# Performance work log

Measured on AMD Instinct MI355X. Metric: run time of the kernel, lower is better.

Reference implementation:

```python
import jax, jax.numpy as jnp
import numpy as np

B, T, C = 2, 2048, 2048
NH, NKV = 16, 4
HD = C // NH  # 128
DFF = 4 * C


def rmsnorm(x):
    eps = jnp.finfo(x.dtype).eps
    return x * jax.lax.rsqrt(jnp.mean(jnp.square(x), axis=-1, keepdims=True) + eps)


def rotary(x, cos, sin):
    # x: [B,T,H,HD], cos/sin: [1,T,1,HD//2]
    d = x.shape[-1] // 2
    x1, x2 = x[..., :d], x[..., d:]
    return jnp.concatenate([x1 * cos + x2 * sin, -x1 * sin + x2 * cos], axis=-1)


def setup_inputs() -> dict:
    key = jax.random.key(0)
    ks = jax.random.split(key, 8)
    x = jax.random.normal(ks[0], (B, T, C), jnp.float32)
    inv_freq = 1.0 / (10000.0 ** (jnp.arange(HD // 2, dtype=jnp.float32) / (HD // 2)))
    ang = jnp.arange(T, dtype=jnp.float32)[:, None] * inv_freq[None, :]  # [T, HD//2]
    cos = jnp.cos(ang)[None, :, None, :]
    sin = jnp.sin(ang)[None, :, None, :]
    s = 0.02
    wq = jax.random.normal(ks[1], (C, NH * HD), jnp.float32) * s
    wk = jax.random.normal(ks[2], (C, NKV * HD), jnp.float32) * s
    wv = jax.random.normal(ks[3], (C, NKV * HD), jnp.float32) * s
    wo = jax.random.normal(ks[4], (C, C), jnp.float32) * s
    w_fc = jax.random.normal(ks[5], (C, DFF), jnp.float32) * s
    w_proj = jax.random.normal(ks[6], (DFF, C), jnp.float32) * s
    return {"x": x, "cos": cos, "sin": sin, "wq": wq, "wk": wk, "wv": wv,
            "wo": wo, "w_fc": w_fc, "w_proj": w_proj}


def reference(x, cos, sin, wq, wk, wv, wo, w_fc, w_proj):
    # --- attention sublayer (pre-norm residual) ---
    h = rmsnorm(x)
    q = (h @ wq).reshape(B, T, NH, HD)
    k = (h @ wk).reshape(B, T, NKV, HD)
    v = (h @ wv).reshape(B, T, NKV, HD)
    q = rmsnorm(rotary(q, cos, sin))
    k = rmsnorm(rotary(k, cos, sin))
    rep = NH // NKV
    k = jnp.repeat(k, rep, axis=2)  # [B,T,NH,HD]
    v = jnp.repeat(v, rep, axis=2)
    scale = 1.0 / np.sqrt(HD)
    scores = jnp.einsum('bqhd,bkhd->bhqk', q, k) * scale
    causal = jnp.tril(jnp.ones((T, T), dtype=bool))
    scores = jnp.where(causal[None, None], scores, jnp.finfo(scores.dtype).min)
    attn = jax.nn.softmax(scores, axis=-1)
    y = jnp.einsum('bhqk,bkhd->bqhd', attn, v).reshape(B, T, C)
    x = x + y @ wo
    # --- MLP sublayer (relu^2) ---
    h = rmsnorm(x)
    h = jnp.square(jax.nn.relu(h @ w_fc))
    x = x + h @ w_proj
    return x
```

## Files before the change

### kernel.cpp

```cpp
#include <hip/hip_runtime.h>
#include <cstdint>
#include <cstddef>


#define B_    2
#define T_    2048
#define C_    2048
#define NH_   16
#define NKV_  4
#define HD_   128
#define DFF_  8192
#define EPS_  1.1920928955078125e-07f

typedef short          bf16x8 __attribute__((ext_vector_type(8)));
typedef float          f32x4  __attribute__((ext_vector_type(4)));
typedef unsigned short u16;
typedef unsigned short u16x8  __attribute__((ext_vector_type(8)));
typedef unsigned short u16x4  __attribute__((ext_vector_type(4)));

__device__ __forceinline__ u16 f2bf(float f) {
    unsigned u = __float_as_uint(f);
    unsigned r = u + 0x7fffu + ((u >> 16) & 1u);
    return (u16)(r >> 16);
}
__device__ __forceinline__ float bf2f(u16 u) {
    return __uint_as_float((unsigned)u << 16);
}

__device__ __forceinline__ void load_lds16(const void* g, void* l) {
    __builtin_amdgcn_global_load_lds(
        (__attribute__((address_space(1))) void*)(g),
        (__attribute__((address_space(3))) void*)(l), 16, 0, 0);
}

__device__ __forceinline__ unsigned lds_addr(const void* p) {
    return (unsigned)(unsigned long long)(__attribute__((address_space(3))) const void*)p;
}

struct TD  { const float* src; u16* dst; int K, N, boff; };
struct TD6 { TD t[6]; };

__global__ void transpose_cast_all(TD6 d) {
    int bid = blockIdx.x;
    int di = 0;
    for (int i = 5; i > 0; --i) if (bid >= d.t[i].boff) { di = i; break; }
    const float* src = d.t[di].src;
    u16* dst = d.t[di].dst;
    int K = d.t[di].K, N = d.t[di].N;
    int lb = bid - d.t[di].boff;
    int nx = N >> 5;
    int n0 = (lb % nx) * 32;
    int k0 = (lb / nx) * 32;

    __shared__ float tile[32][33];
    int tx = threadIdx.x & 31;
    int ty = threadIdx.x >> 5;
    for (int j = 0; j < 4; ++j)
        tile[ty + j * 8][tx] = src[(size_t)(k0 + ty + j * 8) * N + n0 + tx];
    __syncthreads();
    for (int j = 0; j < 4; ++j)
        dst[(size_t)(n0 + ty + j * 8) * K + k0 + tx] = f2bf(tile[tx][ty + j * 8]);
}

__global__ void transpose_v(const u16* __restrict__ vb, u16* __restrict__ Vt) {
    int bx   = blockIdx.x;
    int dblk = bx & 1;
    int t0   = (bx >> 1) * 32;
    int kvh  = blockIdx.y, b = blockIdx.z;
    int dl   = threadIdx.x & 63;
    int tc   = threadIdx.x >> 6;
    int d    = dblk * 64 + dl;
    u16x8 v8;
    for (int j = 0; j < 8; ++j) {
        int t = t0 + tc * 8 + j;
        v8[j] = vb[((size_t)(b * T_ + t) * NKV_ + kvh) * HD_ + d];
    }
    *(u16x8*)(Vt + ((size_t)((b * NKV_ + kvh) * HD_ + d)) * T_ + t0 + tc * 8) = v8;
}

__global__ void rmsnorm_rows(const float* __restrict__ x, u16* __restrict__ out) {
    int row = blockIdx.x;
    const float4* xr = (const float4*)(x + (size_t)row * C_);
    float4 a = xr[threadIdx.x];
    float4 b = xr[threadIdx.x + 256];
    float ss = a.x * a.x + a.y * a.y + a.z * a.z + a.w * a.w
             + b.x * b.x + b.y * b.y + b.z * b.z + b.w * b.w;
    for (int m = 1; m < 64; m <<= 1) ss += __shfl_xor(ss, m, 64);
    __shared__ float part[4];
    if ((threadIdx.x & 63) == 0) part[threadIdx.x >> 6] = ss;
    __syncthreads();
    float tot = part[0] + part[1] + part[2] + part[3];
    float sc = rsqrtf(tot * (1.0f / C_) + EPS_);
    u16x4 o1, o2;
    o1[0] = f2bf(a.x * sc); o1[1] = f2bf(a.y * sc); o1[2] = f2bf(a.z * sc); o1[3] = f2bf(a.w * sc);
    o2[0] = f2bf(b.x * sc); o2[1] = f2bf(b.y * sc); o2[2] = f2bf(b.z * sc); o2[3] = f2bf(b.w * sc);
    u16x4* orow = (u16x4*)(out + (size_t)row * C_);
    orow[threadIdx.x]       = o1;
    orow[threadIdx.x + 256] = o2;
}

__global__ void reduce_rms(const float* __restrict__ x, const u16* __restrict__ p0,
                           const u16* __restrict__ p1, float* __restrict__ x2,
                           u16* __restrict__ hout) {
    int row = blockIdx.x;
    const float4* xr = (const float4*)(x + (size_t)row * C_);
    const u16x4* a0 = (const u16x4*)(p0 + (size_t)row * C_);
    const u16x4* a1 = (const u16x4*)(p1 + (size_t)row * C_);
    float4 v[2];
    float ss = 0.f;
    for (int h = 0; h < 2; ++h) {
        int idx = threadIdx.x + h * 256;
        float4 xv = xr[idx];
        u16x4 b0 = a0[idx], b1 = a1[idx];
        v[h].x = xv.x + bf2f(b0[0]) + bf2f(b1[0]);
        v[h].y = xv.y + bf2f(b0[1]) + bf2f(b1[1]);
        v[h].z = xv.z + bf2f(b0[2]) + bf2f(b1[2]);
        v[h].w = xv.w + bf2f(b0[3]) + bf2f(b1[3]);
        ss += v[h].x * v[h].x + v[h].y * v[h].y + v[h].z * v[h].z + v[h].w * v[h].w;
    }
    for (int m = 1; m < 64; m <<= 1) ss += __shfl_xor(ss, m, 64);
    __shared__ float part[4];
    if ((threadIdx.x & 63) == 0) part[threadIdx.x >> 6] = ss;
    __syncthreads();
    float tot = part[0] + part[1] + part[2] + part[3];
    float sc = rsqrtf(tot * (1.0f / C_) + EPS_);
    float4* x2r = (float4*)(x2 + (size_t)row * C_);
    u16x4* hr   = (u16x4*)(hout + (size_t)row * C_);
    for (int h = 0; h < 2; ++h) {
        int idx = threadIdx.x + h * 256;
        x2r[idx] = v[h];
        u16x4 o;
        o[0] = f2bf(v[h].x * sc); o[1] = f2bf(v[h].y * sc);
        o[2] = f2bf(v[h].z * sc); o[3] = f2bf(v[h].w * sc);
        hr[idx] = o;
    }
}

__global__ void reduce_out(const float* __restrict__ x2, const u16* __restrict__ p0,
                           const u16* __restrict__ p1, float* __restrict__ out) {
    size_t i = (size_t)blockIdx.x * 256 + threadIdx.x;
    float4 xv = ((const float4*)x2)[i];
    u16x4 b0 = ((const u16x4*)p0)[i];
    u16x4 b1 = ((const u16x4*)p1)[i];
    float4 o;
    o.x = xv.x + bf2f(b0[0]) + bf2f(b1[0]);
    o.y = xv.y + bf2f(b0[1]) + bf2f(b1[1]);
    o.z = xv.z + bf2f(b0[2]) + bf2f(b1[2]);
    o.w = xv.w + bf2f(b0[3]) + bf2f(b1[3]);
    ((float4*)out)[i] = o;
}

__global__ void rope_rms2(const float* __restrict__ Xq, const float* __restrict__ Xk,
                          const float* __restrict__ cosb, const float* __restrict__ sinb,
                          u16* __restrict__ Oq, u16* __restrict__ Ok) {
    int gw   = (int)((blockIdx.x * blockDim.x + threadIdx.x) >> 6);
    int lane = threadIdx.x & 63;
    const float* X; u16* O; int t;
    if (gw < B_ * T_ * NH_) {
        X = Xq + (size_t)gw * HD_;  O = Oq + (size_t)gw * HD_;  t = (gw / NH_) % T_;
    } else {
        int w2 = gw - B_ * T_ * NH_;
        X = Xk + (size_t)w2 * HD_;  O = Ok + (size_t)w2 * HD_;  t = (w2 / NKV_) % T_;
    }
    float x1 = X[lane];
    float x2 = X[64 + lane];
    float c  = cosb[t * 64 + lane];
    float sn = sinb[t * 64 + lane];
    float r1 = x1 * c + x2 * sn;
    float r2 = x2 * c - x1 * sn;
    float ss = r1 * r1 + r2 * r2;
    for (int m = 1; m < 64; m <<= 1) ss += __shfl_xor(ss, m, 64);
    float sc = rsqrtf(ss * (1.0f / HD_) + EPS_);
    O[lane]      = f2bf(r1 * sc);
    O[64 + lane] = f2bf(r2 * sc);
}


#define BARRIER() do { __builtin_amdgcn_s_barrier();                     \
                       asm volatile("" ::: "memory"); } while (0)
#define LGKMN(N)  do { asm volatile("s_waitcnt lgkmcnt(" #N ")" ::: "memory");\
                       __builtin_amdgcn_sched_barrier(0); } while (0)

#define DSR(dst, base, lit)                                              \
    asm volatile("ds_read_b128 %0, %1 offset:" lit : "=v"(dst) : "v"(base))

#define READ_AFL() do {                                                  \
    DSR(afl[0][0], aB0, "0");     DSR(afl[0][1], aB1, "0");              \
    DSR(afl[1][0], aB0, "2048");  DSR(afl[1][1], aB1, "2048");           \
    DSR(afl[2][0], aB0, "4096");  DSR(afl[2][1], aB1, "4096");           \
    DSR(afl[3][0], aB0, "6144");  DSR(afl[3][1], aB1, "6144"); } while (0)

#define READ_AFH() do {                                                  \
    DSR(afh[0][0], aB0, "8192");  DSR(afh[0][1], aB1, "8192");           \
    DSR(afh[1][0], aB0, "10240"); DSR(afh[1][1], aB1, "10240");          \
    DSR(afh[2][0], aB0, "12288"); DSR(afh[2][1], aB1, "12288");          \
    DSR(afh[3][0], aB0, "14336"); DSR(afh[3][1], aB1, "14336"); } while (0)

#define READ_BL() do {                                                   \
    DSR(bl[0][0], bB0, "0");     DSR(bl[0][1], bB1, "0");                \
    DSR(bl[1][0], bB0, "2048");  DSR(bl[1][1], bB1, "2048"); } while (0)

#define READ_BH() do {                                                   \
    DSR(bh[0][0], bB0, "4096");  DSR(bh[0][1], bB1, "4096");             \
    DSR(bh[1][0], bB0, "6144");  DSR(bh[1][1], bB1, "6144"); } while (0)

#define MFMA_BLK(AF, BF, MB, NB)                                             \
    _Pragma("unroll")                                                        \
    for (int ks = 0; ks < 2; ++ks)                                           \
        _Pragma("unroll")                                                    \
        for (int mi = 0; mi < 4; ++mi)                                       \
            _Pragma("unroll")                                                \
            for (int ni = 0; ni < 2; ++ni)                                   \
                acc[MB + mi][NB + ni] =                                      \
                    __builtin_amdgcn_mfma_f32_16x16x32_bf16(                 \
                        AF[mi][ks], BF[ni][ks], acc[MB + mi][NB + ni], 0, 0, 0);

template <int EPI>
__launch_bounds__(512, 1)
__global__ void gemm256(const u16* __restrict__ A, const u16* __restrict__ Bt,
                        void* __restrict__ out, void* __restrict__ out2,
                        void* __restrict__ out3, int M, int N, int K, int Ks) {
    __shared__ __attribute__((aligned(16))) u16 sh[65536];

    int tid  = threadIdx.x;
    int l    = tid & 63;
    int w    = tid >> 6;
    int l16  = l & 15;
    int quad = l >> 4;
    int sw   = l & 7;
    int wm   = w >> 2, wn = w & 3;

    int nwg = gridDim.x * gridDim.y;
    int id  = blockIdx.y * gridDim.x + blockIdx.x;
    int sid = (id & 7) * (nwg >> 3) + (id >> 3);
    int bn  = sid % gridDim.x;
    int bm  = sid / gridDim.x;

    size_t koff = (size_t)blockIdx.z * K;
    int nt = K >> 6;

    int csrc = ((l & 7) ^ ((l >> 3) & 7)) * 8;
    int srow = w * 8 + (l >> 3);
    const u16* Ast = A  + (size_t)(bm * 256 + srow) * Ks + koff + csrc;
    const u16* Bst = Bt + (size_t)(bn * 256 + srow) * Ks + koff + csrc;

    auto stageA = [&](int h, int kk, int buf) {
        const u16* g = Ast + (size_t)(h * 128) * Ks + kk;
        u16* d = sh + buf * 32768 + h * 8192 + w * 512;
        load_lds16(g, d);
        load_lds16(g + (size_t)64 * Ks, d + 4096);
    };
    auto stageB = [&](int h, int kk, int buf) {
        const u16* g = Bst + (size_t)(h * 128) * Ks + kk;
        u16* d = sh + buf * 32768 + (2 + h) * 8192 + w * 512;
        load_lds16(g, d);
        load_lds16(g + (size_t)64 * Ks, d + 4096);
    };

    f32x4 acc[8][4];
#pragma unroll
    for (int m = 0; m < 8; ++m)
#pragma unroll
        for (int n = 0; n < 4; ++n) acc[m][n] = (f32x4){0.f, 0.f, 0.f, 0.f};

    stageB(0, 0, 0); stageA(0, 0, 0); stageA(1, 0, 0); stageB(1, 0, 0);
    stageB(0, 64, 1); stageA(0, 64, 1);
    asm volatile("s_waitcnt vmcnt(4)" ::: "memory");
    BARRIER();

    bf16x8 afl[4][2], afh[4][2], bl[2][2], bh[2][2];
    unsigned shbase = lds_addr(sh);
    unsigned ck0 = (unsigned)((quad ^ sw) * 16);
    unsigned ck1 = ck0 ^ 64u;
    unsigned Aoff = (unsigned)(wm * 16384 + l16 * 128);
    unsigned Boff = (unsigned)((2 + (wn >> 1)) * 16384 + (wn & 1) * 8192
                               + l16 * 128);
    unsigned aB0c = shbase + Aoff + ck0, aB1c = shbase + Aoff + ck1;
    unsigned bB0c = shbase + Boff + ck0, bB1c = shbase + Boff + ck1;

    for (int t = 0; t < nt; ++t) {
        int buf = t & 1;
        unsigned bo  = (unsigned)buf << 16;
        unsigned aB0 = aB0c + bo, aB1 = aB1c + bo;
        unsigned bB0 = bB0c + bo, bB1 = bB1c + bo;
        bool s1 = (t + 1 < nt), s2 = (t + 2 < nt);

        READ_AFL();
        READ_BL();
        READ_BH();
        READ_AFH();
        if (s1) { stageA(1, (t + 1) * 64, buf ^ 1);
                  stageB(1, (t + 1) * 64, buf ^ 1); }

        LGKMN(12);
        __builtin_amdgcn_s_setprio(1);
        MFMA_BLK(afl, bl, 0, 0);
        __builtin_amdgcn_s_setprio(0);

        LGKMN(8);
        __builtin_amdgcn_s_setprio(1);
        MFMA_BLK(afl, bh, 0, 2);
        __builtin_amdgcn_s_setprio(0);

        LGKMN(0);
        BARRIER();
        if (s2) { stageB(0, (t + 2) * 64, buf);
                  stageA(0, (t + 2) * 64, buf); }

        __builtin_amdgcn_s_setprio(1);
        MFMA_BLK(afh, bl, 4, 0);
        MFMA_BLK(afh, bh, 4, 2);
        __builtin_amdgcn_s_setprio(0);

        if (s2)      asm volatile("s_waitcnt vmcnt(4)" ::: "memory");
        else if (s1) asm volatile("s_waitcnt vmcnt(0)" ::: "memory");
        BARRIER();
    }

#pragma unroll
    for (int m = 0; m < 8; ++m)
#pragma unroll
        for (int n = 0; n < 4; ++n)
#pragma unroll
            for (int r = 0; r < 4; ++r) {
                int rg = bm * 256 + wm * 128 + m * 16 + quad * 4 + r;
                int cg = bn * 256 + wn * 64 + n * 16 + l16;
                float v = acc[m][n][r];
                if (EPI == 2) {
                    float tv = fmaxf(v, 0.f);
                    ((u16*)out)[(size_t)rg * N + cg] = f2bf(tv * tv);
                } else if (EPI == 4) {
                    if (cg < 2048)      ((float*)out)[(size_t)rg * 2048 + cg] = v;
                    else if (cg < 2560) ((float*)out2)[(size_t)rg * 512 + (cg - 2048)] = v;
                    else                ((u16*)out3)[(size_t)rg * 512 + (cg - 2560)] = f2bf(v);
                } else {
                    u16* p = (blockIdx.z == 0) ? (u16*)out : (u16*)out2;
                    p[(size_t)rg * N + cg] = f2bf(v);
                }
            }
}

__launch_bounds__(256, 2)
__global__ void flash_attn2(const u16* __restrict__ Q, const u16* __restrict__ Kb,
                            const u16* __restrict__ Vt, u16* __restrict__ Y) {
    __shared__ __attribute__((aligned(16))) u16 Qs[128 * 128];
    __shared__ __attribute__((aligned(16))) u16 Ks[64 * 128];
    __shared__ __attribute__((aligned(16))) u16 Vs[128 * 64];

    int bid = blockIdx.x;
    int half = bid >> 8, idx = bid & 255;
    int qr = idx & 15;
    int qt = half ? (15 - qr) : qr;
    int bh = (idx >> 4) | (half << 4);
    int b = bh >> 4, h = bh & 15;
    int kvh = h >> 2;
    int q0 = qt * 128;

    int tid = threadIdx.x, lane = tid & 63, wave = tid >> 6;
    int quad = lane >> 4, l16 = lane & 15;

    {
        int r = lane >> 4;
        for (int c = 0; c < 8; ++c) {
            int row = wave * 32 + c * 4 + r;
            int cc = ((lane & 15) ^ (row & 15)) * 8;
            const u16* g = Q + ((size_t)((b * T_ + q0 + row) * NH_ + h)) * HD_ + cc;
            load_lds16(g, &Qs[(wave * 32 + c * 4) * 128]);
        }
    }
    __syncthreads();

    bf16x8 qf[2][4];
    for (int qtile = 0; qtile < 2; ++qtile)
        for (int kd = 0; kd < 4; ++kd)
            qf[qtile][kd] = *(const bf16x8*)&Qs[(wave * 32 + qtile * 16 + l16) * 128
                                               + (((kd * 4 + quad) ^ l16) * 8)];
    u16* Ps = &Qs[wave * 32 * 128];

    f32x4 zero = {0.f, 0.f, 0.f, 0.f};
    f32x4 o[2][8];
    for (int qtile = 0; qtile < 2; ++qtile)
        for (int dt = 0; dt < 8; ++dt) o[qtile][dt] = zero;
    float m_i[2] = {-__builtin_inff(), -__builtin_inff()};
    float l_i[2] = {0.f, 0.f};
    const float s2s = 0.08838834764831845f * 1.4426950408889634f;

    int nkt = 2 * qt + 2;
    for (int kt = 0; kt < nkt; ++kt) {
        __syncthreads();
        {
            int r = lane >> 4;
            for (int c = 0; c < 4; ++c) {
                int row = wave * 16 + c * 4 + r;
                int cc = ((lane & 15) ^ (row & 15)) * 8;
                const u16* g = Kb + ((size_t)((b * T_ + kt * 64 + row) * NKV_ + kvh)) * HD_ + cc;
                load_lds16(g, &Ks[(wave * 16 + c * 4) * 128]);
            }
        }
        {
            int dr = lane >> 3;
            int kc = (((lane & 7) ^ dr)) * 8;
            for (int c = 0; c < 4; ++c) {
                int drow = wave * 32 + c * 8 + dr;
                const u16* g = Vt + ((size_t)((b * NKV_ + kvh) * HD_ + drow)) * T_ + kt * 64 + kc;
                load_lds16(g, &Vs[(wave * 32 + c * 8) * 64]);
            }
        }
        __syncthreads();

        f32x4 st[2][4];
        for (int qtile = 0; qtile < 2; ++qtile)
            for (int tn = 0; tn < 4; ++tn) st[qtile][tn] = zero;
        for (int tn = 0; tn < 4; ++tn)
            for (int kd = 0; kd < 4; ++kd) {
                bf16x8 kf = *(const bf16x8*)&Ks[(tn * 16 + l16) * 128
                                                + (((kd * 4 + quad) ^ l16) * 8)];
                st[0][tn] = __builtin_amdgcn_mfma_f32_16x16x32_bf16(kf, qf[0][kd], st[0][tn], 0, 0, 0);
                st[1][tn] = __builtin_amdgcn_mfma_f32_16x16x32_bf16(kf, qf[1][kd], st[1][tn], 0, 0, 0);
            }

        for (int qtile = 0; qtile < 2; ++qtile) {
            int qmin = q0 + wave * 32 + qtile * 16;
            int qg   = qmin + l16;
            bool need_mask = (kt * 64 + 63 > qmin);
            float mx = -__builtin_inff();
            for (int tn = 0; tn < 4; ++tn)
                for (int r = 0; r < 4; ++r) {
                    float v = st[qtile][tn][r] * s2s;
                    if (need_mask) {
                        int key = kt * 64 + tn * 16 + quad * 4 + r;
                        if (key > qg) v = -__builtin_inff();
                    }
                    st[qtile][tn][r] = v;
                    mx = fmaxf(mx, v);
                }
            mx = fmaxf(mx, __shfl_xor(mx, 16, 64));
            mx = fmaxf(mx, __shfl_xor(mx, 32, 64));
            float mnew = fmaxf(m_i[qtile], mx);
            float al   = exp2f(m_i[qtile] - mnew);
            m_i[qtile] = mnew;
            float sum = 0.f;
            for (int tn = 0; tn < 4; ++tn) {
                u16x4 pk;
                for (int r = 0; r < 4; ++r) {
                    float e = exp2f(st[qtile][tn][r] - mnew);
                    sum += e;
                    pk[r] = f2bf(e);
                }
                *(u16x4*)&Ps[(qtile * 16 + l16) * 72 + tn * 16 + quad * 4] = pk;
            }
            sum += __shfl_xor(sum, 16, 64);
            sum += __shfl_xor(sum, 32, 64);
            l_i[qtile] = l_i[qtile] * al + sum;
            float aB[4];
            for (int r = 0; r < 4; ++r) aB[r] = __shfl(al, quad * 4 + r, 64);
            for (int dt = 0; dt < 8; ++dt)
                for (int r = 0; r < 4; ++r) o[qtile][dt][r] *= aB[r];
        }

        bf16x8 pf[2][2];
        for (int qtile = 0; qtile < 2; ++qtile)
            for (int ks = 0; ks < 2; ++ks)
                pf[qtile][ks] = *(const bf16x8*)&Ps[(qtile * 16 + l16) * 72 + ks * 32 + quad * 8];
        for (int ks = 0; ks < 2; ++ks)
            for (int dt = 0; dt < 8; ++dt) {
                bf16x8 vf = *(const bf16x8*)&Vs[(dt * 16 + l16) * 64
                                                + (((ks * 4 + quad) ^ (l16 & 7)) * 8)];
                o[0][dt] = __builtin_amdgcn_mfma_f32_16x16x32_bf16(pf[0][ks], vf, o[0][dt], 0, 0, 0);
                o[1][dt] = __builtin_amdgcn_mfma_f32_16x16x32_bf16(pf[1][ks], vf, o[1][dt], 0, 0, 0);
            }
    }

    for (int qtile = 0; qtile < 2; ++qtile) {
        float inv = 1.0f / l_i[qtile];
        float iB[4];
        for (int r = 0; r < 4; ++r) iB[r] = __shfl(inv, quad * 4 + r, 64);
        for (int r = 0; r < 4; ++r) {
            int qg = q0 + wave * 32 + qtile * 16 + quad * 4 + r;
            u16* yr = Y + ((size_t)((b * T_ + qg) * NH_ + h)) * HD_;
            for (int dt = 0; dt < 8; ++dt)
                yr[dt * 16 + l16] = f2bf(o[qtile][dt][r] * iB[r]);
        }
    }
}

extern "C" void kernel_launch(void* const* d_in, const int* in_sizes, int n_in,
                              void* d_out, int out_size, void* d_ws, size_t ws_size,
                              hipStream_t stream) {
    const float* x     = (const float*)d_in[0];
    const float* cosb  = (const float*)d_in[1];
    const float* sinb  = (const float*)d_in[2];
    const float* wq    = (const float*)d_in[3];
    const float* wk    = (const float*)d_in[4];
    const float* wv    = (const float*)d_in[5];
    const float* wo    = (const float*)d_in[6];
    const float* wfc   = (const float*)d_in[7];
    const float* wproj = (const float*)d_in[8];

    char* ws = (char*)d_ws;
    size_t off = 0;
    auto alloc = [&](size_t bytes) { char* p = ws + off; off += (bytes + 255) & ~(size_t)255; return p; };

    u16*   wqkvT  = (u16*)alloc((size_t)3072 * C_ * 2);
    u16*   woT    = (u16*)alloc((size_t)C_ * C_ * 2);
    u16*   wfcT   = (u16*)alloc((size_t)DFF_ * C_ * 2);
    u16*   wprojT = (u16*)alloc((size_t)C_ * DFF_ * 2);
    u16*   hbuf   = (u16*)alloc((size_t)B_ * T_ * C_ * 2);
    float* x2     = (float*)alloc((size_t)B_ * T_ * C_ * 4);
    u16*   ybuf   = (u16*)alloc((size_t)B_ * T_ * C_ * 2);
    u16*   Vtb    = (u16*)alloc((size_t)B_ * NKV_ * HD_ * T_ * 2);
    char*  scratch = alloc((size_t)B_ * T_ * DFF_ * 2);
    float* q_tmp  = (float*)scratch;
    float* k_tmp  = (float*)(scratch + (size_t)B_ * T_ * C_ * 4);
    u16*   qb     = (u16*)(scratch + (size_t)B_ * T_ * C_ * 4 + (size_t)B_ * T_ * 512 * 4);
    u16*   kb     = (u16*)((char*)qb + (size_t)B_ * T_ * C_ * 2);
    u16*   vb     = (u16*)((char*)kb + (size_t)B_ * T_ * 512 * 2);
    u16*   wop1   = (u16*)scratch;
    u16*   ffbuf  = (u16*)scratch;

    const int M = B_ * T_;
    dim3 tb(256);

    TD6 td;
    td.t[0] = { wq,    wqkvT,                       C_,   C_,   0 };
    td.t[1] = { wk,    wqkvT + (size_t)2048 * C_,   C_,   512,  4096 };
    td.t[2] = { wv,    wqkvT + (size_t)2560 * C_,   C_,   512,  5120 };
    td.t[3] = { wo,    woT,                         C_,   C_,   6144 };
    td.t[4] = { wfc,   wfcT,                        C_,   DFF_, 10240 };
    td.t[5] = { wproj, wprojT,                      DFF_, C_,   26624 };
    transpose_cast_all<<<dim3(43008), tb, 0, stream>>>(td);

    rmsnorm_rows<<<M, tb, 0, stream>>>(x, hbuf);

    gemm256<4><<<dim3(3072 / 256, M / 256), dim3(512), 0, stream>>>(
        hbuf, wqkvT, q_tmp, k_tmp, vb, M, 3072, C_, C_);

    rope_rms2<<<dim3((B_ * T_ * (NH_ + NKV_)) / 4), tb, 0, stream>>>(q_tmp, k_tmp, cosb, sinb, qb, kb);
    transpose_v<<<dim3(128, NKV_, B_), tb, 0, stream>>>(vb, Vtb);

    flash_attn2<<<dim3(512), tb, 0, stream>>>(qb, kb, Vtb, ybuf);

    gemm256<5><<<dim3(C_ / 256, M / 256, 2), dim3(512), 0, stream>>>(
        ybuf, woT, hbuf, wop1, nullptr, M, C_, C_ / 2, C_);

    reduce_rms<<<M, tb, 0, stream>>>(x, hbuf, wop1, x2, hbuf);

    gemm256<2><<<dim3(DFF_ / 256, M / 256), dim3(512), 0, stream>>>(
        hbuf, wfcT, ffbuf, nullptr, nullptr, M, DFF_, C_, C_);

    gemm256<5><<<dim3(C_ / 256, M / 256, 2), dim3(512), 0, stream>>>(
        ffbuf, wprojT, hbuf, ybuf, nullptr, M, C_, DFF_ / 2, DFF_);

    reduce_out<<<dim3((M * C_) / 1024), tb, 0, stream>>>(x2, hbuf, ybuf, (float*)d_out);
}
```

Before: 703.0 us.

## Prefetch next-tile LDS fragments during current MFMA blocks in GEMM main loop

Restructures the double-buffered GEMM loop so the LDS fragment reads for tile t+1 are issued while tile t's MFMA blocks still execute, with fragments preloaded before the loop. Global-to-LDS staging now loads whole tiles two steps ahead instead of splitting halves across iterations. MFMA block order and barrier/waitcnt placement change to match. The aim is to hide LDS read latency behind matrix math, at the cost of more live registers, a full vmcnt(0) wait each iteration, and more delicate barrier correctness.

```diff
diff --git a/kernel.cpp b/kernel.cpp
--- a/kernel.cpp
+++ b/kernel.cpp
@@ -184,25 +184,25 @@
 #define DSR(dst, base, lit)                                              \
     asm volatile("ds_read_b128 %0, %1 offset:" lit : "=v"(dst) : "v"(base))
 
-#define READ_AFL() do {                                                  \
-    DSR(afl[0][0], aB0, "0");     DSR(afl[0][1], aB1, "0");              \
-    DSR(afl[1][0], aB0, "2048");  DSR(afl[1][1], aB1, "2048");           \
-    DSR(afl[2][0], aB0, "4096");  DSR(afl[2][1], aB1, "4096");           \
-    DSR(afl[3][0], aB0, "6144");  DSR(afl[3][1], aB1, "6144"); } while (0)
-
-#define READ_AFH() do {                                                  \
-    DSR(afh[0][0], aB0, "8192");  DSR(afh[0][1], aB1, "8192");           \
-    DSR(afh[1][0], aB0, "10240"); DSR(afh[1][1], aB1, "10240");          \
-    DSR(afh[2][0], aB0, "12288"); DSR(afh[2][1], aB1, "12288");          \
-    DSR(afh[3][0], aB0, "14336"); DSR(afh[3][1], aB1, "14336"); } while (0)
-
-#define READ_BL() do {                                                   \
-    DSR(bl[0][0], bB0, "0");     DSR(bl[0][1], bB1, "0");                \
-    DSR(bl[1][0], bB0, "2048");  DSR(bl[1][1], bB1, "2048"); } while (0)
-
-#define READ_BH() do {                                                   \
-    DSR(bh[0][0], bB0, "4096");  DSR(bh[0][1], bB1, "4096");             \
-    DSR(bh[1][0], bB0, "6144");  DSR(bh[1][1], bB1, "6144"); } while (0)
+#define READ_AFL(a0, a1) do {                                            \
+    DSR(afl[0][0], a0, "0");     DSR(afl[0][1], a1, "0");                \
+    DSR(afl[1][0], a0, "2048");  DSR(afl[1][1], a1, "2048");             \
+    DSR(afl[2][0], a0, "4096");  DSR(afl[2][1], a1, "4096");             \
+    DSR(afl[3][0], a0, "6144");  DSR(afl[3][1], a1, "6144"); } while (0)
+
+#define READ_AFH(a0, a1) do {                                            \
+    DSR(afh[0][0], a0, "8192");  DSR(afh[0][1], a1, "8192");             \
+    DSR(afh[1][0], a0, "10240"); DSR(afh[1][1], a1, "10240");            \
+    DSR(afh[2][0], a0, "12288"); DSR(afh[2][1], a1, "12288");            \
+    DSR(afh[3][0], a0, "14336"); DSR(afh[3][1], a1, "14336"); } while (0)
+
+#define READ_BL(b0, b1) do {                                             \
+    DSR(bl[0][0], b0, "0");     DSR(bl[0][1], b1, "0");                  \
+    DSR(bl[1][0], b0, "2048");  DSR(bl[1][1], b1, "2048"); } while (0)
+
+#define READ_BH(b0, b1) do {                                             \
+    DSR(bh[0][0], b0, "4096");  DSR(bh[0][1], b1, "4096");               \
+    DSR(bh[1][0], b0, "6144");  DSR(bh[1][1], b1, "6144"); } while (0)
 
 #define MFMA_BLK(AF, BF, MB, NB)                                             \
     _Pragma("unroll")                                                        \
@@ -263,11 +263,6 @@
 #pragma unroll
         for (int n = 0; n < 4; ++n) acc[m][n] = (f32x4){0.f, 0.f, 0.f, 0.f};
 
-    stageB(0, 0, 0); stageA(0, 0, 0); stageA(1, 0, 0); stageB(1, 0, 0);
-    stageB(0, 64, 1); stageA(0, 64, 1);
-    asm volatile("s_waitcnt vmcnt(4)" ::: "memory");
-    BARRIER();
-
     bf16x8 afl[4][2], afh[4][2], bl[2][2], bh[2][2];
     unsigned shbase = lds_addr(sh);
     unsigned ck0 = (unsigned)((quad ^ sw) * 16);
@@ -278,43 +273,51 @@
     unsigned aB0c = shbase + Aoff + ck0, aB1c = shbase + Aoff + ck1;
     unsigned bB0c = shbase + Boff + ck0, bB1c = shbase + Boff + ck1;
 
+    stageB(0, 0, 0); stageA(0, 0, 0); stageA(1, 0, 0); stageB(1, 0, 0);
+    asm volatile("s_waitcnt vmcnt(0)" ::: "memory");
+    BARRIER();
+    READ_BL(bB0c, bB1c);
+    READ_AFL(aB0c, aB1c);
+    READ_AFH(aB0c, aB1c);
+    READ_BH(bB0c, bB1c);
+    if (nt > 1) { stageB(0, 64, 1); stageA(0, 64, 1);
+                  stageA(1, 64, 1); stageB(1, 64, 1); }
+
     for (int t = 0; t < nt; ++t) {
         int buf = t & 1;
-        unsigned bo  = (unsigned)buf << 16;
-        unsigned aB0 = aB0c + bo, aB1 = aB1c + bo;
-        unsigned bB0 = bB0c + bo, bB1 = bB1c + bo;
+        unsigned nbo  = (unsigned)(buf ^ 1) << 16;
+        unsigned aB0n = aB0c + nbo, aB1n = aB1c + nbo;
+        unsigned bB0n = bB0c + nbo, bB1n = bB1c + nbo;
         bool s1 = (t + 1 < nt), s2 = (t + 2 < nt);
-
-        READ_AFL();
-        READ_BL();
-        READ_BH();
-        READ_AFH();
-        if (s1) { stageA(1, (t + 1) * 64, buf ^ 1);
-                  stageB(1, (t + 1) * 64, buf ^ 1); }
 
         LGKMN(12);
         __builtin_amdgcn_s_setprio(1);
         MFMA_BLK(afl, bl, 0, 0);
         __builtin_amdgcn_s_setprio(0);
 
-        LGKMN(8);
+        LGKMN(4);
+        __builtin_amdgcn_s_setprio(1);
+        MFMA_BLK(afh, bl, 4, 0);
+        __builtin_amdgcn_s_setprio(0);
+
+        asm volatile("s_waitcnt vmcnt(0)" ::: "memory");
+        BARRIER();
+        if (s1) READ_BL(bB0n, bB1n);
+
+        if (s1) { LGKMN(4); } else { LGKMN(0); }
         __builtin_amdgcn_s_setprio(1);
         MFMA_BLK(afl, bh, 0, 2);
         __builtin_amdgcn_s_setprio(0);
 
-        LGKMN(0);
         BARRIER();
-        if (s2) { stageB(0, (t + 2) * 64, buf);
-                  stageA(0, (t + 2) * 64, buf); }
+        if (s2) { stageB(0, (t + 2) * 64, buf); stageA(0, (t + 2) * 64, buf);
+                  stageA(1, (t + 2) * 64, buf); stageB(1, (t + 2) * 64, buf); }
+        if (s1) READ_AFL(aB0n, aB1n);
 
         __builtin_amdgcn_s_setprio(1);
-        MFMA_BLK(afh, bl, 4, 0);
         MFMA_BLK(afh, bh, 4, 2);
         __builtin_amdgcn_s_setprio(0);
-
-        if (s2)      asm volatile("s_waitcnt vmcnt(4)" ::: "memory");
-        else if (s1) asm volatile("s_waitcnt vmcnt(0)" ::: "memory");
-        BARRIER();
+        if (s1) { READ_AFH(aB0n, aB1n); READ_BH(bB0n, bB1n); }
     }
 
 #pragma unroll
```

Result: slower. 732.2 us (+4.2%).
